# Optimization experiments

Measured on AMD Instinct MI355X. Metric: run time of the kernel, lower is better.

The kernel has to match this reference:

```python
import jax, jax.numpy as jnp
import numpy as np

N_NODES = 50000
N_EDGES = 800000
D_IN = 512
D_HID = 64
D_OUT = 40


def setup_inputs() -> dict:
    key = jax.random.key(0)
    ks = jax.random.split(key, 8)
    x = jax.random.normal(ks[0], (N_NODES, D_IN), dtype=jnp.float32)
    edge_index = jax.random.randint(ks[1], (2, N_EDGES), 0, N_NODES, dtype=jnp.int32)
    w_mul = jax.random.uniform(ks[2], (N_EDGES,), dtype=jnp.float32)
    s1 = 1.0 / np.sqrt(D_IN)
    s2 = 1.0 / np.sqrt(D_HID)
    W1 = jax.random.uniform(ks[3], (D_IN, D_HID), minval=-s1, maxval=s1, dtype=jnp.float32)
    b1 = jax.random.uniform(ks[4], (D_HID,), minval=-s1, maxval=s1, dtype=jnp.float32)
    W2 = jax.random.uniform(ks[5], (D_HID, D_OUT), minval=-s2, maxval=s2, dtype=jnp.float32)
    b2 = jax.random.uniform(ks[6], (D_OUT,), minval=-s2, maxval=s2, dtype=jnp.float32)
    return {"x": x, "edge_index": edge_index, "w_mul": w_mul,
            "W1": W1, "b1": b1, "W2": W2, "b2": b2}


def _conv(h, src, dst, w_mul, W, b, n_nodes):
    # linear transform, then gather-scale-scatter-add (PyG aggr='add')
    h = h @ W + b                      # [N, d_out]
    msg = w_mul[:, None] * h[src]      # [E, d_out] gather + scale
    return jax.ops.segment_sum(msg, dst, num_segments=n_nodes)  # scatter-add


def reference(x, edge_index, w_mul, W1, b1, W2, b2):
    n_nodes = x.shape[0]
    src, dst = edge_index[0], edge_index[1]  # flow: source_to_target
    h = _conv(x, src, dst, w_mul, W1, b1, n_nodes)
    h = jax.nn.relu(h)
    h = _conv(h, src, dst, w_mul, W2, b2, n_nodes)
    return jax.nn.log_softmax(h, axis=1)
```

## Files before the change

kernel.cpp:

```cpp
#include <hip/hip_runtime.h>
#include <math.h>

#define D_IN  512
#define D_HID 64
#define D_OUT 40
#define CAP   64

typedef __attribute__((ext_vector_type(8))) short bf16x8;
typedef __attribute__((ext_vector_type(4))) float f32x4;

static __device__ __forceinline__ unsigned short f2bf(float f) {
    unsigned u = __float_as_uint(f);
    return (unsigned short)((u + 0x7FFF + ((u >> 16) & 1)) >> 16);
}
static __device__ __forceinline__ float bf2f(unsigned short h) {
    return __uint_as_float(((unsigned)h) << 16);
}

__global__ __launch_bounds__(256)
void prep_all(int* __restrict__ cursor, const float* __restrict__ W1,
              unsigned short* __restrict__ w1T, const float* __restrict__ W2,
              unsigned short* __restrict__ w2T, int N) {
    const int i = blockIdx.x * blockDim.x + threadIdx.x;
    if (i < N) cursor[i] = 0;
    const int j = i - N;
    if (j >= 0 && j < D_IN * D_HID) {
        const int k = j >> 6, col = j & 63;
        w1T[col * D_IN + k] = f2bf(W1[j]);
    }
    const int l = j - D_IN * D_HID;
    if (l >= 0 && l < 48 * D_HID) {
        const int col = l >> 6, k = l & 63;
        w2T[l] = (col < D_OUT) ? f2bf(W2[k * D_OUT + col]) : 0;
    }
}

__global__ __launch_bounds__(256)
void fat1(const float* __restrict__ x, const unsigned short* __restrict__ w1T,
          const float* __restrict__ b1, unsigned short* __restrict__ h1,
          const int* __restrict__ src, const int* __restrict__ dstA,
          const float* __restrict__ wm, int* __restrict__ cursor,
          unsigned* __restrict__ edges, int E, int N, int sBlocks) {
    __shared__ unsigned char lds[16384];
    const int t = threadIdx.x;

    if ((int)blockIdx.x < sBlocks) {
        const int slice = (N + 7) >> 3;
        const int lo = (blockIdx.x & 7) * slice;
        const int hi = min(N, lo + slice);
        const int nChunk = sBlocks >> 3;
        const int per = (E + nChunk - 1) / nChunk;
        const int beg = ((int)blockIdx.x >> 3) * per;
        const int end = min(E, beg + per);
        for (int e = beg + t; e < end; e += 256) {
            const int d = dstA[e];
            if (d >= lo && d < hi) {
                const int pos = atomicAdd(&cursor[d], 1);
                if (pos < CAP)
                    edges[(size_t)d * CAP + pos] =
                        ((unsigned)src[e] << 16) | (unsigned)f2bf(wm[e]);
            }
        }
        return;
    }

    const int lane = t & 63;
    const int wv = t >> 6;
    const int nodeBase = ((int)blockIdx.x - sBlocks) * 64;

    f32x4 acc[4];
#pragma unroll
    for (int cg = 0; cg < 4; ++cg) acc[cg] = (f32x4){0.f, 0.f, 0.f, 0.f};

    for (int k0 = 0; k0 < D_IN; k0 += 64) {
#pragma unroll
        for (int hh = 0; hh < 2; ++hh) {
            const int g = t + hh * 256;
            const int row = g >> 3, slot = g & 7;
            int gn = nodeBase + row; if (gn >= N) gn = N - 1;
            const float* sp = x + (size_t)gn * D_IN + k0 + slot * 8;
            const float4 a = *reinterpret_cast<const float4*>(sp);
            const float4 b = *reinterpret_cast<const float4*>(sp + 4);
            uint4 p;
            p.x = (unsigned)f2bf(a.x) | ((unsigned)f2bf(a.y) << 16);
            p.y = (unsigned)f2bf(a.z) | ((unsigned)f2bf(a.w) << 16);
            p.z = (unsigned)f2bf(b.x) | ((unsigned)f2bf(b.y) << 16);
            p.w = (unsigned)f2bf(b.z) | ((unsigned)f2bf(b.w) << 16);
            *reinterpret_cast<uint4*>(lds + row * 128 + ((slot << 4) ^ ((row & 7) << 4))) = p;
        }
#pragma unroll
        for (int hh = 0; hh < 2; ++hh) {
            const int g = t + hh * 256;
            const int col = g >> 3, slot = g & 7;
            const uint4 p = *reinterpret_cast<const uint4*>(w1T + (size_t)col * D_IN + k0 + slot * 8);
            *reinterpret_cast<uint4*>(lds + 8192 + col * 128 + ((slot << 4) ^ ((col & 7) << 4))) = p;
        }
        __syncthreads();

        const int fr = lane & 15;
        const int fc = lane >> 4;
#pragma unroll
        for (int s = 0; s < 2; ++s) {
            const int slot = s * 4 + fc;
            const int arow = wv * 16 + fr;
            const bf16x8 afrag = *reinterpret_cast<const bf16x8*>(
                lds + arow * 128 + ((slot << 4) ^ ((arow & 7) << 4)));
#pragma unroll
            for (int cg = 0; cg < 4; ++cg) {
                const int brow = cg * 16 + fr;
                const bf16x8 bfrag = *reinterpret_cast<const bf16x8*>(
                    lds + 8192 + brow * 128 + ((slot << 4) ^ ((brow & 7) << 4)));
                acc[cg] = __builtin_amdgcn_mfma_f32_16x16x32_bf16(afrag, bfrag, acc[cg], 0, 0, 0);
            }
        }
        __syncthreads();
    }

    const int fr = lane & 15;
    const int rq = lane >> 4;
#pragma unroll
    for (int cg = 0; cg < 4; ++cg) {
        const int col = cg * 16 + fr;
        const float bb = b1[col];
#pragma unroll
        for (int r = 0; r < 4; ++r) {
            const int node = nodeBase + wv * 16 + rq * 4 + r;
            if (node < N)
                h1[(size_t)node * D_HID + col] = f2bf(acc[cg][r] + bb);
        }
    }
}

__global__ __launch_bounds__(256)
void agg_hid(const unsigned short* __restrict__ h, const unsigned* __restrict__ edges,
             const int* __restrict__ count, unsigned short* __restrict__ agg1, int N) {
    const int lane = threadIdx.x & 63;
    const int wv   = (threadIdx.x >> 6);
    const int slice = (N + 7) >> 3;
    const int local = ((int)blockIdx.x >> 3) * 4 + wv;
    if (local >= slice) return;
    const int n = ((int)blockIdx.x & 7) * slice + local;
    if (n >= N) return;
    const unsigned er = edges[(size_t)n * CAP + lane];
    const int cnt = min(count[n], CAP);
    float acc = 0.f;
    int j = 0;
    for (; j + 8 <= cnt; j += 8) {
        unsigned p[8];
#pragma unroll
        for (int u = 0; u < 8; ++u) p[u] = (unsigned)__shfl((int)er, j + u);
        float v[8];
#pragma unroll
        for (int u = 0; u < 8; ++u) v[u] = bf2f(h[(size_t)(p[u] >> 16) * D_HID + lane]);
#pragma unroll
        for (int u = 0; u < 8; ++u)
            acc += bf2f((unsigned short)(p[u] & 0xffff)) * v[u];
    }
    for (; j < cnt; ++j) {
        const unsigned p0 = (unsigned)__shfl((int)er, j);
        acc += bf2f((unsigned short)(p0 & 0xffff)) *
               bf2f(h[(size_t)(p0 >> 16) * D_HID + lane]);
    }
    agg1[(size_t)n * D_HID + lane] = f2bf(fmaxf(acc, 0.f));
}

__global__ __launch_bounds__(256)
void gemm2_mfma(const unsigned short* __restrict__ agg1,
                const unsigned short* __restrict__ w2T,
                const float* __restrict__ b2, unsigned short* __restrict__ h2, int N) {
    __shared__ unsigned char lds[8192 + 6144];
    const int t = threadIdx.x;
    const int lane = t & 63;
    const int wv = t >> 6;
    const int nodeBase = blockIdx.x * 64;

#pragma unroll
    for (int hh = 0; hh < 2; ++hh) {
        const int g = t + hh * 256;
        const int row = g >> 3, slot = g & 7;
        int gn = nodeBase + row; if (gn >= N) gn = N - 1;
        const uint4 p = *reinterpret_cast<const uint4*>(agg1 + (size_t)gn * D_HID + slot * 8);
        *reinterpret_cast<uint4*>(lds + row * 128 + ((slot << 4) ^ ((row & 7) << 4))) = p;
    }
    for (int g = t; g < 384; g += 256) {
        const int row = g >> 3, slot = g & 7;
        const uint4 p = *reinterpret_cast<const uint4*>(w2T + (size_t)row * D_HID + slot * 8);
        *reinterpret_cast<uint4*>(lds + 8192 + row * 128 + ((slot << 4) ^ ((row & 7) << 4))) = p;
    }
    __syncthreads();

    f32x4 acc[3];
#pragma unroll
    for (int cg = 0; cg < 3; ++cg) acc[cg] = (f32x4){0.f, 0.f, 0.f, 0.f};

    const int fr = lane & 15;
    const int fc = lane >> 4;
#pragma unroll
    for (int s = 0; s < 2; ++s) {
        const int slot = s * 4 + fc;
        const int arow = wv * 16 + fr;
        const bf16x8 afrag = *reinterpret_cast<const bf16x8*>(
            lds + arow * 128 + ((slot << 4) ^ ((arow & 7) << 4)));
#pragma unroll
        for (int cg = 0; cg < 3; ++cg) {
            const int brow = cg * 16 + fr;
            const bf16x8 bfrag = *reinterpret_cast<const bf16x8*>(
                lds + 8192 + brow * 128 + ((slot << 4) ^ ((brow & 7) << 4)));
            acc[cg] = __builtin_amdgcn_mfma_f32_16x16x32_bf16(afrag, bfrag, acc[cg], 0, 0, 0);
        }
    }

    const int rq = lane >> 4;
#pragma unroll
    for (int cg = 0; cg < 3; ++cg) {
        const int col = cg * 16 + fr;
        if (col < D_OUT) {
            const float bb = b2[col];
#pragma unroll
            for (int r = 0; r < 4; ++r) {
                const int node = nodeBase + wv * 16 + rq * 4 + r;
                if (node < N)
                    h2[(size_t)node * D_OUT + col] = f2bf(acc[cg][r] + bb);
            }
        }
    }
}

__global__ __launch_bounds__(256)
void agg40_lsm(const unsigned short* __restrict__ h2, const unsigned* __restrict__ edges,
               const int* __restrict__ count, float* __restrict__ out, int N) {
    const int lane = threadIdx.x & 63;
    const int col  = (lane < D_OUT) ? lane : 0;
    const int wv   = (threadIdx.x >> 6);
    const int slice = (N + 7) >> 3;
    const int local = ((int)blockIdx.x >> 3) * 4 + wv;
    if (local >= slice) return;
    const int n = ((int)blockIdx.x & 7) * slice + local;
    if (n >= N) return;
    const unsigned er = edges[(size_t)n * CAP + lane];
    const int cnt = min(count[n], CAP);
    float acc = 0.f;
    int j = 0;
    for (; j + 8 <= cnt; j += 8) {
        unsigned p[8];
#pragma unroll
        for (int u = 0; u < 8; ++u) p[u] = (unsigned)__shfl((int)er, j + u);
        float v[8];
#pragma unroll
        for (int u = 0; u < 8; ++u) v[u] = bf2f(h2[(size_t)(p[u] >> 16) * D_OUT + col]);
#pragma unroll
        for (int u = 0; u < 8; ++u)
            acc += bf2f((unsigned short)(p[u] & 0xffff)) * v[u];
    }
    for (; j < cnt; ++j) {
        const unsigned p0 = (unsigned)__shfl((int)er, j);
        acc += bf2f((unsigned short)(p0 & 0xffff)) *
               bf2f(h2[(size_t)(p0 >> 16) * D_OUT + col]);
    }
    const float v = (lane < D_OUT) ? acc : -INFINITY;
    float m = v;
#pragma unroll
    for (int o = 32; o > 0; o >>= 1) m = fmaxf(m, __shfl_xor(m, o, 64));
    float s = (lane < D_OUT) ? __expf(v - m) : 0.f;
#pragma unroll
    for (int o = 32; o > 0; o >>= 1) s += __shfl_xor(s, o, 64);
    if (lane < D_OUT) out[(size_t)n * D_OUT + lane] = v - m - __logf(s);
}

extern "C" void kernel_launch(void* const* d_in, const int* in_sizes, int n_in,
                              void* d_out, int out_size, void* d_ws, size_t ws_size,
                              hipStream_t stream) {
    const float* x   = (const float*)d_in[0];
    const int*   ei  = (const int*)d_in[1];
    const float* wm  = (const float*)d_in[2];
    const float* W1  = (const float*)d_in[3];
    const float* b1  = (const float*)d_in[4];
    const float* W2  = (const float*)d_in[5];
    const float* b2  = (const float*)d_in[6];

    const int N = in_sizes[0] / D_IN;
    const int E = in_sizes[2];
    const int* srcIdx = ei;
    const int* dstIdx = ei + E;

    unsigned short* w1T    = (unsigned short*)d_ws;
    unsigned short* h1bf   = w1T + (size_t)D_HID * D_IN;
    unsigned short* agg1bf = h1bf + (size_t)N * D_HID;
    unsigned* edges        = (unsigned*)(agg1bf + (size_t)N * D_HID);
    int*   cursor          = (int*)(edges + (size_t)N * CAP);
    unsigned short* w2T    = (unsigned short*)(cursor + N);
    unsigned short* h2bf   = h1bf;
    float* out             = (float*)d_out;

    const int g1Blocks = (N + 63) / 64;
    const int sBlocks  = 1024;
    const int prepWork = N + D_IN * D_HID + 48 * D_HID;
    const int slice = (N + 7) >> 3;
    const int aggBlocks = ((slice + 3) / 4) * 8;

    prep_all<<<(prepWork + 255) / 256, 256, 0, stream>>>(cursor, W1, w1T, W2, w2T, N);
    fat1<<<sBlocks + g1Blocks, 256, 0, stream>>>(
        x, w1T, b1, h1bf, srcIdx, dstIdx, wm, cursor, edges, E, N, sBlocks);
    agg_hid<<<aggBlocks, 256, 0, stream>>>(h1bf, edges, cursor, agg1bf, N);
    gemm2_mfma<<<g1Blocks, 256, 0, stream>>>(agg1bf, w2T, b2, h2bf, N);
    agg40_lsm<<<aggBlocks, 256, 0, stream>>>(h2bf, edges, cursor, out, N);
}
```

Baseline: 116.4 us.

## Widen fat1 K-step to 256 and issue global loads into registers before LDS sync

The fat1 GEMM now processes K in two 256-wide chunks instead of eight 64-wide chunks. It loads 8 float4 pairs of x and 8 uint4 of W1T per thread into registers before the barrier, so loads for the next chunk overlap compute on the previous one. This means fewer barriers and more memory-level parallelism. The cost is LDS growing from 16KB to 64KB plus many more live registers, which may cut occupancy, and the 64KB LDS is also allocated for the scatter blocks.

Result: slower. 150.2 us (+29.0%).

```diff
diff --git a/kernel.cpp b/kernel.cpp
--- a/kernel.cpp
+++ b/kernel.cpp
@@ -41,7 +41,7 @@
           const int* __restrict__ src, const int* __restrict__ dstA,
           const float* __restrict__ wm, int* __restrict__ cursor,
           unsigned* __restrict__ edges, int E, int N, int sBlocks) {
-    __shared__ unsigned char lds[16384];
+    __shared__ unsigned char lds[65536];
     const int t = threadIdx.x;
 
     if ((int)blockIdx.x < sBlocks) {
@@ -67,56 +67,67 @@
     const int lane = t & 63;
     const int wv = t >> 6;
     const int nodeBase = ((int)blockIdx.x - sBlocks) * 64;
+    const int fr = lane & 15;
+    const int fc = lane >> 4;
 
     f32x4 acc[4];
 #pragma unroll
     for (int cg = 0; cg < 4; ++cg) acc[cg] = (f32x4){0.f, 0.f, 0.f, 0.f};
 
-    for (int k0 = 0; k0 < D_IN; k0 += 64) {
-#pragma unroll
-        for (int hh = 0; hh < 2; ++hh) {
-            const int g = t + hh * 256;
-            const int row = g >> 3, slot = g & 7;
+    for (int kbase = 0; kbase < D_IN; kbase += 256) {
+        float4 xa[8], xb[8];
+        uint4  wr[8];
+#pragma unroll
+        for (int i = 0; i < 8; ++i) {
+            const int G = t + i * 256;
+            const int row = G >> 5, g = G & 31;
             int gn = nodeBase + row; if (gn >= N) gn = N - 1;
-            const float* sp = x + (size_t)gn * D_IN + k0 + slot * 8;
-            const float4 a = *reinterpret_cast<const float4*>(sp);
-            const float4 b = *reinterpret_cast<const float4*>(sp + 4);
+            const float* sp = x + (size_t)gn * D_IN + kbase + g * 8;
+            xa[i] = *reinterpret_cast<const float4*>(sp);
+            xb[i] = *reinterpret_cast<const float4*>(sp + 4);
+        }
+#pragma unroll
+        for (int i = 0; i < 8; ++i) {
+            const int G = t + i * 256;
+            const int col = G >> 5, g = G & 31;
+            wr[i] = *reinterpret_cast<const uint4*>(w1T + (size_t)col * D_IN + kbase + g * 8);
+        }
+        if (kbase) __syncthreads();
+#pragma unroll
+        for (int i = 0; i < 8; ++i) {
+            const int G = t + i * 256;
+            const int row = G >> 5, g = G & 31;
             uint4 p;
-            p.x = (unsigned)f2bf(a.x) | ((unsigned)f2bf(a.y) << 16);
-            p.y = (unsigned)f2bf(a.z) | ((unsigned)f2bf(a.w) << 16);
-            p.z = (unsigned)f2bf(b.x) | ((unsigned)f2bf(b.y) << 16);
-            p.w = (unsigned)f2bf(b.z) | ((unsigned)f2bf(b.w) << 16);
-            *reinterpret_cast<uint4*>(lds + row * 128 + ((slot << 4) ^ ((row & 7) << 4))) = p;
-        }
-#pragma unroll
-        for (int hh = 0; hh < 2; ++hh) {
-            const int g = t + hh * 256;
-            const int col = g >> 3, slot = g & 7;
-            const uint4 p = *reinterpret_cast<const uint4*>(w1T + (size_t)col * D_IN + k0 + slot * 8);
-            *reinterpret_cast<uint4*>(lds + 8192 + col * 128 + ((slot << 4) ^ ((col & 7) << 4))) = p;
+            p.x = (unsigned)f2bf(xa[i].x) | ((unsigned)f2bf(xa[i].y) << 16);
+            p.y = (unsigned)f2bf(xa[i].z) | ((unsigned)f2bf(xa[i].w) << 16);
+            p.z = (unsigned)f2bf(xb[i].x) | ((unsigned)f2bf(xb[i].y) << 16);
+            p.w = (unsigned)f2bf(xb[i].z) | ((unsigned)f2bf(xb[i].w) << 16);
+            *reinterpret_cast<uint4*>(lds + row * 512 + ((g * 16) ^ ((row & 7) << 4))) = p;
+        }
+#pragma unroll
+        for (int i = 0; i < 8; ++i) {
+            const int G = t + i * 256;
+            const int col = G >> 5, g = G & 31;
+            *reinterpret_cast<uint4*>(lds + 32768 + col * 512 + ((g * 16) ^ ((col & 7) << 4))) = wr[i];
         }
         __syncthreads();
 
-        const int fr = lane & 15;
-        const int fc = lane >> 4;
-#pragma unroll
-        for (int s = 0; s < 2; ++s) {
-            const int slot = s * 4 + fc;
+#pragma unroll
+        for (int s = 0; s < 8; ++s) {
+            const int g = s * 4 + fc;
             const int arow = wv * 16 + fr;
             const bf16x8 afrag = *reinterpret_cast<const bf16x8*>(
-                lds + arow * 128 + ((slot << 4) ^ ((arow & 7) << 4)));
+                lds + arow * 512 + ((g * 16) ^ ((arow & 7) << 4)));
 #pragma unroll
             for (int cg = 0; cg < 4; ++cg) {
                 const int brow = cg * 16 + fr;
                 const bf16x8 bfrag = *reinterpret_cast<const bf16x8*>(
-                    lds + 8192 + brow * 128 + ((slot << 4) ^ ((brow & 7) << 4)));
+                    lds + 32768 + brow * 512 + ((g * 16) ^ ((brow & 7) << 4)));
                 acc[cg] = __builtin_amdgcn_mfma_f32_16x16x32_bf16(afrag, bfrag, acc[cg], 0, 0, 0);
             }
         }
-        __syncthreads();
-    }
-
-    const int fr = lane & 15;
+    }
+
     const int rq = lane >> 4;
 #pragma unroll
     for (int cg = 0; cg < 4; ++cg) {
```

## Shrink fat1 GEMM to single-wave blocks loading MFMA fragments directly from global

Applied to the files above, without the earlier changes.

The first-layer GEMM drops its shared-memory staging and barriers. Each 64-thread block now handles 16 nodes and loads the x and W1 fragments straight from global memory into MFMA registers. The scatter part uses 2048 one-wave blocks instead of 1024 four-wave blocks. This removes LDS traffic and syncs and raises occupancy, but W1 is no longer reused across waves through LDS, and the N bound check on the last tile is removed (fine only when N is a multiple of 16).

New measurement: 143.9 us. 23.6% more time.

```diff
diff --git a/kernel.cpp b/kernel.cpp
--- a/kernel.cpp
+++ b/kernel.cpp
@@ -35,13 +35,12 @@
     }
 }
 
-__global__ __launch_bounds__(256)
+__global__ __launch_bounds__(64)
 void fat1(const float* __restrict__ x, const unsigned short* __restrict__ w1T,
           const float* __restrict__ b1, unsigned short* __restrict__ h1,
           const int* __restrict__ src, const int* __restrict__ dstA,
           const float* __restrict__ wm, int* __restrict__ cursor,
           unsigned* __restrict__ edges, int E, int N, int sBlocks) {
-    __shared__ unsigned char lds[16384];
     const int t = threadIdx.x;
 
     if ((int)blockIdx.x < sBlocks) {
@@ -52,7 +51,7 @@
         const int per = (E + nChunk - 1) / nChunk;
         const int beg = ((int)blockIdx.x >> 3) * per;
         const int end = min(E, beg + per);
-        for (int e = beg + t; e < end; e += 256) {
+        for (int e = beg + t; e < end; e += 64) {
             const int d = dstA[e];
             if (d >= lo && d < hi) {
                 const int pos = atomicAdd(&cursor[d], 1);
@@ -64,59 +63,39 @@
         return;
     }
 
-    const int lane = t & 63;
-    const int wv = t >> 6;
-    const int nodeBase = ((int)blockIdx.x - sBlocks) * 64;
+    const int lane = t;
+    const int fr = lane & 15;
+    const int fc = lane >> 4;
+    const int nodeBase = ((int)blockIdx.x - sBlocks) * 16;
+    const float* xrow = x + (size_t)(nodeBase + fr) * D_IN + fc * 8;
+    const unsigned short* wbase = w1T + fc * 8;
 
     f32x4 acc[4];
 #pragma unroll
     for (int cg = 0; cg < 4; ++cg) acc[cg] = (f32x4){0.f, 0.f, 0.f, 0.f};
 
-    for (int k0 = 0; k0 < D_IN; k0 += 64) {
-#pragma unroll
-        for (int hh = 0; hh < 2; ++hh) {
-            const int g = t + hh * 256;
-            const int row = g >> 3, slot = g & 7;
-            int gn = nodeBase + row; if (gn >= N) gn = N - 1;
-            const float* sp = x + (size_t)gn * D_IN + k0 + slot * 8;
-            const float4 a = *reinterpret_cast<const float4*>(sp);
-            const float4 b = *reinterpret_cast<const float4*>(sp + 4);
-            uint4 p;
-            p.x = (unsigned)f2bf(a.x) | ((unsigned)f2bf(a.y) << 16);
-            p.y = (unsigned)f2bf(a.z) | ((unsigned)f2bf(a.w) << 16);
-            p.z = (unsigned)f2bf(b.x) | ((unsigned)f2bf(b.y) << 16);
-            p.w = (unsigned)f2bf(b.z) | ((unsigned)f2bf(b.w) << 16);
-            *reinterpret_cast<uint4*>(lds + row * 128 + ((slot << 4) ^ ((row & 7) << 4))) = p;
-        }
-#pragma unroll
-        for (int hh = 0; hh < 2; ++hh) {
-            const int g = t + hh * 256;
-            const int col = g >> 3, slot = g & 7;
-            const uint4 p = *reinterpret_cast<const uint4*>(w1T + (size_t)col * D_IN + k0 + slot * 8);
-            *reinterpret_cast<uint4*>(lds + 8192 + col * 128 + ((slot << 4) ^ ((col & 7) << 4))) = p;
-        }
-        __syncthreads();
-
-        const int fr = lane & 15;
-        const int fc = lane >> 4;
+#pragma unroll 2
+    for (int c = 0; c < 8; ++c) {
+        const int kc = c * 64;
 #pragma unroll
         for (int s = 0; s < 2; ++s) {
-            const int slot = s * 4 + fc;
-            const int arow = wv * 16 + fr;
-            const bf16x8 afrag = *reinterpret_cast<const bf16x8*>(
-                lds + arow * 128 + ((slot << 4) ^ ((arow & 7) << 4)));
+            const float4 a = *reinterpret_cast<const float4*>(xrow + kc + s * 32);
+            const float4 b = *reinterpret_cast<const float4*>(xrow + kc + s * 32 + 4);
+            uint4 pk;
+            pk.x = (unsigned)f2bf(a.x) | ((unsigned)f2bf(a.y) << 16);
+            pk.y = (unsigned)f2bf(a.z) | ((unsigned)f2bf(a.w) << 16);
+            pk.z = (unsigned)f2bf(b.x) | ((unsigned)f2bf(b.y) << 16);
+            pk.w = (unsigned)f2bf(b.z) | ((unsigned)f2bf(b.w) << 16);
+            const bf16x8 afrag = *reinterpret_cast<const bf16x8*>(&pk);
 #pragma unroll
             for (int cg = 0; cg < 4; ++cg) {
-                const int brow = cg * 16 + fr;
                 const bf16x8 bfrag = *reinterpret_cast<const bf16x8*>(
-                    lds + 8192 + brow * 128 + ((slot << 4) ^ ((brow & 7) << 4)));
+                    wbase + (size_t)(cg * 16 + fr) * D_IN + kc + s * 32);
                 acc[cg] = __builtin_amdgcn_mfma_f32_16x16x32_bf16(afrag, bfrag, acc[cg], 0, 0, 0);
             }
         }
-        __syncthreads();
-    }
-
-    const int fr = lane & 15;
+    }
+
     const int rq = lane >> 4;
 #pragma unroll
     for (int cg = 0; cg < 4; ++cg) {
@@ -124,9 +103,8 @@
         const float bb = b1[col];
 #pragma unroll
         for (int r = 0; r < 4; ++r) {
-            const int node = nodeBase + wv * 16 + rq * 4 + r;
-            if (node < N)
-                h1[(size_t)node * D_HID + col] = f2bf(acc[cg][r] + bb);
+            const int node = nodeBase + rq * 4 + r;
+            h1[(size_t)node * D_HID + col] = f2bf(acc[cg][r] + bb);
         }
     }
 }
@@ -292,16 +270,17 @@
     unsigned short* h2bf   = h1bf;
     float* out             = (float*)d_out;
 
-    const int g1Blocks = (N + 63) / 64;
-    const int sBlocks  = 1024;
+    const int g1Blocks = (N + 15) / 16;
+    const int sBlocks  = 2048;
+    const int g2Blocks = (N + 63) / 64;
     const int prepWork = N + D_IN * D_HID + 48 * D_HID;
     const int slice = (N + 7) >> 3;
     const int aggBlocks = ((slice + 3) / 4) * 8;
 
     prep_all<<<(prepWork + 255) / 256, 256, 0, stream>>>(cursor, W1, w1T, W2, w2T, N);
-    fat1<<<sBlocks + g1Blocks, 256, 0, stream>>>(
+    fat1<<<sBlocks + g1Blocks, 64, 0, stream>>>(
         x, w1T, b1, h1bf, srcIdx, dstIdx, wm, cursor, edges, E, N, sBlocks);
     agg_hid<<<aggBlocks, 256, 0, stream>>>(h1bf, edges, cursor, agg1bf, N);
-    gemm2_mfma<<<g1Blocks, 256, 0, stream>>>(agg1bf, w2T, b2, h2bf, N);
+    gemm2_mfma<<<g2Blocks, 256, 0, stream>>>(agg1bf, w2T, b2, h2bf, N);
     agg40_lsm<<<aggBlocks, 256, 0, stream>>>(h2bf, edges, cursor, out, N);
 }
```

## Double-buffer LDS in fat1 GEMM and prefetch next K-chunk into registers

Applied to the files above, without the earlier changes.

The first-layer GEMM in fat1 now uses two LDS buffers and loads the next 64-wide K chunk of x and W1 into registers while the current chunk's MFMAs run. It replaces the two __syncthreads per iteration with one barrier after an lgkmcnt wait. The goal is to overlap global load latency with matrix compute. In exchange LDS per block doubles to 32 KB, which may lower occupancy and reduce the latency hiding that came from running more waves.

Result: slower. 123.2 us (+5.8%).

```diff
diff --git a/kernel.cpp b/kernel.cpp
--- a/kernel.cpp
+++ b/kernel.cpp
@@ -41,7 +41,7 @@
           const int* __restrict__ src, const int* __restrict__ dstA,
           const float* __restrict__ wm, int* __restrict__ cursor,
           unsigned* __restrict__ edges, int E, int N, int sBlocks) {
-    __shared__ unsigned char lds[16384];
+    __shared__ unsigned char lds[32768];
     const int t = threadIdx.x;
 
     if ((int)blockIdx.x < sBlocks) {
@@ -67,56 +67,80 @@
     const int lane = t & 63;
     const int wv = t >> 6;
     const int nodeBase = ((int)blockIdx.x - sBlocks) * 64;
+    const int fr = lane & 15;
+    const int fc = lane >> 4;
+
+    const int row0 = t >> 3, slot0 = t & 7;
+    const int row1 = (t + 256) >> 3, slot1 = (t + 256) & 7;
+    int gn0 = nodeBase + row0; if (gn0 >= N) gn0 = N - 1;
+    int gn1 = nodeBase + row1; if (gn1 >= N) gn1 = N - 1;
+    const float* xp0 = x + (size_t)gn0 * D_IN + slot0 * 8;
+    const float* xp1 = x + (size_t)gn1 * D_IN + slot1 * 8;
+    const unsigned short* wp0 = w1T + (size_t)row0 * D_IN + slot0 * 8;
+    const unsigned short* wp1 = w1T + (size_t)row1 * D_IN + slot1 * 8;
 
     f32x4 acc[4];
 #pragma unroll
     for (int cg = 0; cg < 4; ++cg) acc[cg] = (f32x4){0.f, 0.f, 0.f, 0.f};
 
-    for (int k0 = 0; k0 < D_IN; k0 += 64) {
-#pragma unroll
-        for (int hh = 0; hh < 2; ++hh) {
-            const int g = t + hh * 256;
-            const int row = g >> 3, slot = g & 7;
-            int gn = nodeBase + row; if (gn >= N) gn = N - 1;
-            const float* sp = x + (size_t)gn * D_IN + k0 + slot * 8;
-            const float4 a = *reinterpret_cast<const float4*>(sp);
-            const float4 b = *reinterpret_cast<const float4*>(sp + 4);
+    float4 xa0 = *reinterpret_cast<const float4*>(xp0);
+    float4 xb0 = *reinterpret_cast<const float4*>(xp0 + 4);
+    float4 xa1 = *reinterpret_cast<const float4*>(xp1);
+    float4 xb1 = *reinterpret_cast<const float4*>(xp1 + 4);
+    uint4  wr0 = *reinterpret_cast<const uint4*>(wp0);
+    uint4  wr1 = *reinterpret_cast<const uint4*>(wp1);
+
+#pragma unroll 1
+    for (int c = 0; c < 8; ++c) {
+        const int base = (c & 1) << 14;
+
+        {
             uint4 p;
-            p.x = (unsigned)f2bf(a.x) | ((unsigned)f2bf(a.y) << 16);
-            p.y = (unsigned)f2bf(a.z) | ((unsigned)f2bf(a.w) << 16);
-            p.z = (unsigned)f2bf(b.x) | ((unsigned)f2bf(b.y) << 16);
-            p.w = (unsigned)f2bf(b.z) | ((unsigned)f2bf(b.w) << 16);
-            *reinterpret_cast<uint4*>(lds + row * 128 + ((slot << 4) ^ ((row & 7) << 4))) = p;
-        }
-#pragma unroll
-        for (int hh = 0; hh < 2; ++hh) {
-            const int g = t + hh * 256;
-            const int col = g >> 3, slot = g & 7;
-            const uint4 p = *reinterpret_cast<const uint4*>(w1T + (size_t)col * D_IN + k0 + slot * 8);
-            *reinterpret_cast<uint4*>(lds + 8192 + col * 128 + ((slot << 4) ^ ((col & 7) << 4))) = p;
-        }
-        __syncthreads();
-
-        const int fr = lane & 15;
-        const int fc = lane >> 4;
+            p.x = (unsigned)f2bf(xa0.x) | ((unsigned)f2bf(xa0.y) << 16);
+            p.y = (unsigned)f2bf(xa0.z) | ((unsigned)f2bf(xa0.w) << 16);
+            p.z = (unsigned)f2bf(xb0.x) | ((unsigned)f2bf(xb0.y) << 16);
+            p.w = (unsigned)f2bf(xb0.z) | ((unsigned)f2bf(xb0.w) << 16);
+            *reinterpret_cast<uint4*>(lds + base + row0 * 128 + ((slot0 << 4) ^ ((row0 & 7) << 4))) = p;
+            p.x = (unsigned)f2bf(xa1.x) | ((unsigned)f2bf(xa1.y) << 16);
+            p.y = (unsigned)f2bf(xa1.z) | ((unsigned)f2bf(xa1.w) << 16);
+            p.z = (unsigned)f2bf(xb1.x) | ((unsigned)f2bf(xb1.y) << 16);
+            p.w = (unsigned)f2bf(xb1.z) | ((unsigned)f2bf(xb1.w) << 16);
+            *reinterpret_cast<uint4*>(lds + base + row1 * 128 + ((slot1 << 4) ^ ((row1 & 7) << 4))) = p;
+            *reinterpret_cast<uint4*>(lds + base + 8192 + row0 * 128 + ((slot0 << 4) ^ ((row0 & 7) << 4))) = wr0;
+            *reinterpret_cast<uint4*>(lds + base + 8192 + row1 * 128 + ((slot1 << 4) ^ ((row1 & 7) << 4))) = wr1;
+        }
+
+        if (c < 7) {
+            const int kn = (c + 1) * 64;
+            xa0 = *reinterpret_cast<const float4*>(xp0 + kn);
+            xb0 = *reinterpret_cast<const float4*>(xp0 + kn + 4);
+            xa1 = *reinterpret_cast<const float4*>(xp1 + kn);
+            xb1 = *reinterpret_cast<const float4*>(xp1 + kn + 4);
+            wr0 = *reinterpret_cast<const uint4*>(wp0 + kn);
+            wr1 = *reinterpret_cast<const uint4*>(wp1 + kn);
+        }
+
+        asm volatile("s_waitcnt lgkmcnt(0)" ::: "memory");
+        __builtin_amdgcn_sched_barrier(0);
+        __builtin_amdgcn_s_barrier();
+        __builtin_amdgcn_sched_barrier(0);
+
 #pragma unroll
         for (int s = 0; s < 2; ++s) {
             const int slot = s * 4 + fc;
             const int arow = wv * 16 + fr;
             const bf16x8 afrag = *reinterpret_cast<const bf16x8*>(
-                lds + arow * 128 + ((slot << 4) ^ ((arow & 7) << 4)));
+                lds + base + arow * 128 + ((slot << 4) ^ ((arow & 7) << 4)));
 #pragma unroll
             for (int cg = 0; cg < 4; ++cg) {
                 const int brow = cg * 16 + fr;
                 const bf16x8 bfrag = *reinterpret_cast<const bf16x8*>(
-                    lds + 8192 + brow * 128 + ((slot << 4) ^ ((brow & 7) << 4)));
+                    lds + base + 8192 + brow * 128 + ((slot << 4) ^ ((brow & 7) << 4)));
                 acc[cg] = __builtin_amdgcn_mfma_f32_16x16x32_bf16(afrag, bfrag, acc[cg], 0, 0, 0);
             }
         }
-        __syncthreads();
-    }
-
-    const int fr = lane & 15;
+    }
+
     const int rq = lane >> 4;
 #pragma unroll
     for (int cg = 0; cg < 4; ++cg) {
```
